# Optimization experiments

Measured on AMD Instinct MI355X. Metric: run time of the kernel, lower is better.

The kernel has to match this reference:

```python
import jax, jax.numpy as jnp
import numpy as np

B = 512
N_ENT = 100000
N_REL = 64
D = 200          # embed_dim
D1 = 10          # embed_shape (emb_dim1)
D2 = 20          # embed_dim // embed_shape (emb_dim2)
K = 3            # kernel_size
C = 32           # out_channels
FC_IN = C * (2 * D1 - K + 1) * (D2 - K + 1)  # 32*18*18 = 10368
EPS = 1e-5       # BatchNorm eps
LS = 0.1         # label_smoothing
LAM = 1e-5       # kg_l2_loss_lambda


def setup_inputs() -> dict:
    key = jax.random.key(0)
    ks = jax.random.split(key, 8)
    return dict(
        entity_w=jax.random.normal(ks[0], (N_ENT, D), jnp.float32) * 0.1,
        relation_w=jax.random.normal(ks[1], (N_REL, D), jnp.float32) * 0.1,
        conv_w=jax.random.normal(ks[2], (C, 1, K, K), jnp.float32) * 0.1,
        conv_b=jnp.zeros((C,), jnp.float32),
        fc_w=jax.random.normal(ks[3], (D, FC_IN), jnp.float32) * 0.02,
        fc_b=jnp.zeros((D,), jnp.float32),
        b=jnp.zeros((N_ENT,), jnp.float32),
        bn0_g=jnp.ones((1,), jnp.float32), bn0_b=jnp.zeros((1,), jnp.float32),
        bn1_g=jnp.ones((C,), jnp.float32), bn1_b=jnp.zeros((C,), jnp.float32),
        bn2_g=jnp.ones((D,), jnp.float32), bn2_b=jnp.zeros((D,), jnp.float32),
        h=jax.random.randint(ks[4], (B,), 0, N_ENT),
        r=jax.random.randint(ks[5], (B,), 0, N_REL),
        pos_t=jax.random.randint(ks[6], (B,), 0, N_ENT),
    )


def _bn(x, g, b, axes, shape):
    # training-mode batchnorm (batch statistics), biased variance as in torch
    m = jnp.mean(x, axes, keepdims=True)
    v = jnp.var(x, axes, keepdims=True)
    return (x - m) * jax.lax.rsqrt(v + EPS) * g.reshape(shape) + b.reshape(shape)


def _l2_mean(x):
    # torch: mean(sum(x**2, dim=1) / 2)
    return jnp.mean(jnp.sum(x * x, axis=1) / 2.0)


def reference(entity_w, relation_w, conv_w, conv_b, fc_w, fc_b, b,
              bn0_g, bn0_b, bn1_g, bn1_b, bn2_g, bn2_b, h, r, pos_t):
    h_e = entity_w[h].reshape(B, 1, D1, D2)
    r_e = relation_w[r].reshape(B, 1, D1, D2)
    x = jnp.concatenate([h_e, r_e], axis=2)           # [B,1,2*D1,D2]
    x = _bn(x, bn0_g, bn0_b, (0, 2, 3), (1, 1, 1, 1))
    x = jax.lax.conv_general_dilated(
        x, conv_w, (1, 1), 'VALID',
        dimension_numbers=('NCHW', 'OIHW', 'NCHW')) + conv_b.reshape(1, C, 1, 1)
    x = _bn(x, bn1_g, bn1_b, (0, 2, 3), (1, C, 1, 1))
    x = jax.nn.relu(x).reshape(B, -1)                 # [B, FC_IN]
    x = x @ fc_w.T + fc_b                             # [B, D]
    x = _bn(x, bn2_g, bn2_b, (0,), (1, D))
    x = jax.nn.leaky_relu(x)                          # slope 0.01 = torch default
    scores = x @ entity_w.T + b                       # [B, N_ENT]
    # BCEWithLogits with smoothed label y = (1-LS)*onehot(pos_t) + 1/N_ENT,
    # loss = mean(softplus(s) - s*y); one-hot never materialized.
    sp_sum = jnp.sum(jax.nn.softplus(scores))
    xy_sum = jnp.sum(scores) / N_ENT + (1.0 - LS) * jnp.sum(
        scores[jnp.arange(B), pos_t])
    kg_loss = (sp_sum - xy_sum) / (B * N_ENT)
    l2 = _l2_mean(h_e) + _l2_mean(r_e) + _l2_mean(conv_w) + _l2_mean(fc_w)
    return kg_loss + LAM * l2
```

## Files before the change

### kernel.cpp

```cpp
#include <hip/hip_runtime.h>
#include <math.h>

#define NB_B 512
#define NE 100000
#define NE_PAD 100032
#define DD 200
#define CC 32
#define FCIN 10368
#define HW 324
#define BNEPS 1e-5f
#define KP 224

#define ENT_BLKS 10941
#define FCW_BLKS 1013
#define GATH_OFF (ENT_BLKS + FCW_BLKS)

typedef __attribute__((ext_vector_type(8))) short short8;
typedef __attribute__((ext_vector_type(4))) float floatx4;


static __device__ __forceinline__ float blk_reduce(float v, volatile float* sbuf) {
  for (int o = 32; o > 0; o >>= 1) v += __shfl_down(v, o, 64);
  int lane = threadIdx.x & 63, wid = threadIdx.x >> 6;
  if (lane == 0) sbuf[wid] = v;
  __syncthreads();
  float r = 0.f;
  int nw = (blockDim.x + 63) >> 6;
  if ((int)threadIdx.x < nw) r = sbuf[threadIdx.x];
  if (threadIdx.x < 64) {
    for (int o = 32; o > 0; o >>= 1) r += __shfl_down(r, o, 64);
  }
  __syncthreads();
  return r;
}

static __device__ __forceinline__ unsigned short f32_to_bf16(float f) {
  unsigned int u = __float_as_uint(f);
  u += 0x7fffu + ((u >> 16) & 1u);
  return (unsigned short)(u >> 16);
}
static __device__ __forceinline__ float bf16_to_f32(unsigned short b) {
  return __uint_as_float(((unsigned int)b) << 16);
}

__global__ __launch_bounds__(256) void k_cvt(const float* __restrict__ ent,
                                             unsigned short* __restrict__ entb,
                                             const float* __restrict__ fcw,
                                             unsigned short* __restrict__ fcwb,
                                             const float* __restrict__ rel,
                                             const int* __restrict__ h,
                                             const int* __restrict__ r,
                                             float* __restrict__ x0,
                                             double* dacc) {
  if (blockIdx.x < ENT_BLKS) {
    int g = blockIdx.x * 256 + threadIdx.x;
    int row = g / 28;
    int c8 = (g - row * 28) * 8;
    ushort4 o0, o1;
    if (c8 < 200 && row < NE) {
      const float4* s = (const float4*)(ent + (long)row * DD + c8);
      float4 u = s[0], v = s[1];
      o0.x = f32_to_bf16(u.x); o0.y = f32_to_bf16(u.y);
      o0.z = f32_to_bf16(u.z); o0.w = f32_to_bf16(u.w);
      o1.x = f32_to_bf16(v.x); o1.y = f32_to_bf16(v.y);
      o1.z = f32_to_bf16(v.z); o1.w = f32_to_bf16(v.w);
    } else {
      o0.x = o0.y = o0.z = o0.w = 0;
      o1.x = o1.y = o1.z = o1.w = 0;
    }
    ushort4* d = (ushort4*)(entb + (long)row * KP + c8);
    d[0] = o0; d[1] = o1;
  } else if (blockIdx.x < GATH_OFF) {
    int g = (blockIdx.x - ENT_BLKS) * 256 + threadIdx.x;
    float sq = 0.f;
    if (g < 259200) {
      const float4* s = (const float4*)(fcw + (long)g * 8);
      float4 u = s[0], v = s[1];
      sq = u.x*u.x + u.y*u.y + u.z*u.z + u.w*u.w
         + v.x*v.x + v.y*v.y + v.z*v.z + v.w*v.w;
      ushort4 o0, o1;
      o0.x = f32_to_bf16(u.x); o0.y = f32_to_bf16(u.y);
      o0.z = f32_to_bf16(u.z); o0.w = f32_to_bf16(u.w);
      o1.x = f32_to_bf16(v.x); o1.y = f32_to_bf16(v.y);
      o1.z = f32_to_bf16(v.z); o1.w = f32_to_bf16(v.w);
      ushort4* d = (ushort4*)(fcwb + (long)g * 8);
      d[0] = o0; d[1] = o1;
    }
    __shared__ float sbuf[8];
    float tq = blk_reduce(sq, sbuf);
    if (threadIdx.x == 0) atomicAdd(&dacc[67], (double)tq);
  } else {
    int b = blockIdx.x - GATH_OFF;
    int hi = h[b], ri = r[b];
    float s = 0.f, sq = 0.f;
    for (int i = threadIdx.x; i < 400; i += 256) {
      float v = (i < 200) ? ent[(long)hi * DD + i] : rel[(long)ri * DD + (i - 200)];
      x0[b * 400 + i] = v;
      s += v; sq += v * v;
    }
    __shared__ float sbuf[8];
    float ts = blk_reduce(s, sbuf);
    float tq = blk_reduce(sq, sbuf);
    if (threadIdx.x == 0) {
      atomicAdd(&dacc[0], (double)ts);
      atomicAdd(&dacc[1], (double)tq);
    }
  }
}

__global__ __launch_bounds__(256) void k_conv(const float* __restrict__ x0,
                       const float* __restrict__ convw, const float* __restrict__ convb,
                       const float* __restrict__ g0, const float* __restrict__ b0,
                       unsigned short* __restrict__ yb, double* dacc) {
  __shared__ float xs[400], wsm[288], cbs[32], ssum[32], ssq[32];
  __shared__ float a0s, s0s;
  int b = blockIdx.x, t = threadIdx.x;
  for (int i = t; i < 400; i += 256) xs[i] = x0[b * 400 + i];
  for (int i = t; i < 288; i += 256) wsm[i] = convw[i];
  if (t < 32) cbs[t] = convb[t];
  if (t == 0) {
    double m = dacc[0] / 204800.0;
    double v = dacc[1] / 204800.0 - m * m;
    float a = g0[0] * rsqrtf((float)v + BNEPS);
    a0s = a; s0s = b0[0] - (float)m * a;
  }
  __syncthreads();
  float a0 = a0s, s0 = s0s;
  for (int i = t; i < 400; i += 256) xs[i] = a0 * xs[i] + s0;
  __syncthreads();
  int c = t >> 3, sub = t & 7;
  const float* w = &wsm[c * 9];
  float cb = cbs[c];
  float s = 0.f, sq = 0.f;
  for (int e = sub; e < HW; e += 8) {
    int oh = e / 18, ow = e - oh * 18;
    const float* xp = &xs[oh * 20 + ow];
    float acc = cb
       + xp[0] * w[0] + xp[1] * w[1] + xp[2] * w[2]
       + xp[20] * w[3] + xp[21] * w[4] + xp[22] * w[5]
       + xp[40] * w[6] + xp[41] * w[7] + xp[42] * w[8];
    yb[(long)b * FCIN + c * HW + e] = f32_to_bf16(acc);
    s += acc; sq += acc * acc;
  }
  s += __shfl_xor(s, 1, 64); sq += __shfl_xor(sq, 1, 64);
  s += __shfl_xor(s, 2, 64); sq += __shfl_xor(sq, 2, 64);
  s += __shfl_xor(s, 4, 64); sq += __shfl_xor(sq, 4, 64);
  if (sub == 0) { ssum[c] = s; ssq[c] = sq; }
  __syncthreads();
  if (t < 32) {
    atomicAdd(&dacc[2 + t], (double)ssum[t]);
    atomicAdd(&dacc[34 + t], (double)ssq[t]);
  }
}

__global__ __launch_bounds__(256) void k_prep(unsigned short* __restrict__ yb,
                                              const float* __restrict__ g1,
                                              const float* __restrict__ b1,
                                              const double* __restrict__ dacc) {
  __shared__ float a1s[32], sh1s[32];
  int t = threadIdx.x;
  if (t < 32) {
    double cnt = 512.0 * 324.0;
    double m = dacc[2 + t] / cnt, v = dacc[34 + t] / cnt - m * m;
    float a = g1[t] * rsqrtf((float)v + BNEPS);
    a1s[t] = a; sh1s[t] = b1[t] - (float)m * a;
  }
  __syncthreads();
  int g = blockIdx.x * 256 + t;
  int row = g / 1296;
  int c8 = (g - row * 1296) * 8;
  unsigned short* p = yb + (long)row * FCIN + c8;
  ushort4 v0 = ((ushort4*)p)[0], v1 = ((ushort4*)p)[1];
  unsigned short e[8] = {v0.x, v0.y, v0.z, v0.w, v1.x, v1.y, v1.z, v1.w};
#pragma unroll
  for (int j = 0; j < 8; j++) {
    int c = (c8 + j) / HW;
    float f = a1s[c] * bf16_to_f32(e[j]) + sh1s[c];
    e[j] = f32_to_bf16(fmaxf(f, 0.f));
  }
  v0.x = e[0]; v0.y = e[1]; v0.z = e[2]; v0.w = e[3];
  v1.x = e[4]; v1.y = e[5]; v1.z = e[6]; v1.w = e[7];
  ((ushort4*)p)[0] = v0; ((ushort4*)p)[1] = v1;
}

__global__ __launch_bounds__(64) void k_fc3(const unsigned short* __restrict__ yb,
                                            const unsigned short* __restrict__ fcwb,
                                            float* __restrict__ Cp) {
  int wid = blockIdx.x;
  int ks = wid >> 5, rem = wid & 31;
  int mt = rem >> 2, nt = rem & 3;
  int m0 = mt * 64, n0 = nt * 64;
  int lane = threadIdx.x;
  int quad = lane >> 4, lr = lane & 15;
  long kbeg = (long)ks * 864;

  const unsigned short* arow[4];
  const unsigned short* brow[4];
#pragma unroll
  for (int mi = 0; mi < 4; mi++)
    arow[mi] = yb + (long)(m0 + mi * 16 + lr) * FCIN + kbeg + quad * 8;
#pragma unroll
  for (int ni = 0; ni < 4; ni++) {
    int d = n0 + ni * 16 + lr;
    if (d > DD - 1) d = DD - 1;
    brow[ni] = fcwb + (long)d * FCIN + kbeg + quad * 8;
  }

  floatx4 acc[4][4];
#pragma unroll
  for (int i = 0; i < 4; i++)
#pragma unroll
    for (int j = 0; j < 4; j++) acc[i][j] = (floatx4){0.f, 0.f, 0.f, 0.f};

  short8 sA[3][4], sB[3][4];
#pragma unroll
  for (int c = 0; c < 3; c++) {
#pragma unroll
    for (int mi = 0; mi < 4; mi++) sA[c][mi] = *(const short8*)(arow[mi] + c * 32);
#pragma unroll
    for (int ni = 0; ni < 4; ni++) sB[c][ni] = *(const short8*)(brow[ni] + c * 32);
  }
  for (int c3 = 0; c3 < 9; c3++) {
    int cc = c3 * 3;
#pragma unroll
    for (int j = 0; j < 3; j++) {
#pragma unroll
      for (int ni = 0; ni < 4; ni++)
#pragma unroll
        for (int mi = 0; mi < 4; mi++)
          acc[mi][ni] = __builtin_amdgcn_mfma_f32_16x16x32_bf16(sA[j][mi], sB[j][ni], acc[mi][ni], 0, 0, 0);
      int nxt = cc + j + 3;
      if (nxt < 27) {
#pragma unroll
        for (int mi = 0; mi < 4; mi++) sA[j][mi] = *(const short8*)(arow[mi] + nxt * 32);
#pragma unroll
        for (int ni = 0; ni < 4; ni++) sB[j][ni] = *(const short8*)(brow[ni] + nxt * 32);
      }
    }
  }

  float* out = Cp + (long)ks * (NB_B * DD);
#pragma unroll
  for (int ni = 0; ni < 4; ni++) {
    int d = n0 + ni * 16 + lr;
    if (d < DD) {
#pragma unroll
      for (int mi = 0; mi < 4; mi++) {
        int mbase = m0 + mi * 16 + quad * 4;
#pragma unroll
        for (int rg = 0; rg < 4; rg++)
          out[(mbase + rg) * DD + d] = acc[mi][ni][rg];
      }
    }
  }
}

__global__ __launch_bounds__(256) void k_fcred(const float* __restrict__ Cp,
                                               float* __restrict__ Cfc) {
  int g = blockIdx.x * 256 + threadIdx.x;
  float4 s = ((const float4*)Cp)[g];
#pragma unroll
  for (int p = 1; p < 12; p++) {
    float4 v = ((const float4*)(Cp + (long)p * (NB_B * DD)))[g];
    s.x += v.x; s.y += v.y; s.z += v.z; s.w += v.w;
  }
  ((float4*)Cfc)[g] = s;
}

__global__ void k_bn2stats(const float* __restrict__ Cfc, const float* __restrict__ fcb,
                           const float* __restrict__ g2, const float* __restrict__ b2,
                           float* __restrict__ a2, float* __restrict__ b2c) {
  int d = blockIdx.x, lane = threadIdx.x;
  float s = 0.f, sq = 0.f;
  for (int b = lane; b < NB_B; b += 64) {
    float v = Cfc[b * DD + d] + fcb[d];
    s += v; sq += v * v;
  }
  for (int o = 32; o > 0; o >>= 1) { s += __shfl_down(s, o, 64); sq += __shfl_down(sq, o, 64); }
  if (lane == 0) {
    float m = s / 512.f, v = sq / 512.f - m * m;
    float a = g2[d] * rsqrtf(v + BNEPS);
    a2[d] = a; b2c[d] = b2[d] - m * a;
  }
}

__global__ __launch_bounds__(256) void k_xfinal(const float* __restrict__ Cfc,
                         const float* __restrict__ fcb,
                         const float* __restrict__ a2, const float* __restrict__ b2c,
                         const float* __restrict__ ent, const float* __restrict__ bias,
                         const int* __restrict__ pos,
                         float* __restrict__ xf, unsigned short* __restrict__ xfb,
                         double* dacc) {
  __shared__ float xs[224];
  __shared__ float sbuf[8];
  int b = blockIdx.x, t = threadIdx.x;
  if (t < KP) {
    float xv = 0.f;
    if (t < DD) {
      float v = Cfc[b * DD + t] + fcb[t];
      xv = a2[t] * v + b2c[t];
      xv = xv >= 0.f ? xv : 0.01f * xv;
      xf[b * DD + t] = xv;
    }
    xfb[b * KP + t] = f32_to_bf16(xv);
    xs[t] = xv;
  }
  __syncthreads();
  int e = pos[b];
  float s = (t < DD) ? xs[t] * ent[(long)e * DD + t] : 0.f;
  float ts = blk_reduce(s, sbuf);
  if (t == 0) atomicAdd(&dacc[70], (double)(ts + bias[e]));
}

__global__ __launch_bounds__(512) void k_scores4(
    const unsigned short* __restrict__ entb,
    const unsigned short* __restrict__ xfb,
    const float* __restrict__ bias, double* dacc) {
  __shared__ float sbuf[8];
  int t = threadIdx.x;
  int wv = t >> 6, lane = t & 63;
  int quad = lane >> 4, lr = lane & 15;

  short8 af[4][7];
#pragma unroll
  for (int mi = 0; mi < 4; mi++) {
    const unsigned short* ap = xfb + (size_t)(wv * 64 + mi * 16 + lr) * KP + quad * 8;
#pragma unroll
    for (int kc = 0; kc < 7; kc++) af[mi][kc] = *(const short8*)(ap + kc * 32);
  }

  float sp = 0.f, ss = 0.f;
  int t0 = blockIdx.x * 3;
#pragma unroll 1
  for (int tile = t0; tile < t0 + 3; tile++) {
    int e0 = tile * 64;
    const unsigned short* bp[4];
    float b4[4];
#pragma unroll
    for (int ni = 0; ni < 4; ni++) {
      int e = e0 + ni * 16 + lr;
      int ec = e < NE ? e : (NE - 1);
      bp[ni] = entb + (size_t)e * KP + quad * 8;
      float bv = bias[ec];
      b4[ni] = (e < NE) ? bv : 0.f;
    }
    floatx4 acc[4][4];
#pragma unroll
    for (int i = 0; i < 4; i++)
#pragma unroll
      for (int j = 0; j < 4; j++) acc[i][j] = (floatx4){0.f, 0.f, 0.f, 0.f};

    short8 bs[2][4];
#pragma unroll
    for (int ni = 0; ni < 4; ni++) bs[0][ni] = *(const short8*)(bp[ni]);
#pragma unroll
    for (int ni = 0; ni < 4; ni++) bs[1][ni] = *(const short8*)(bp[ni] + 32);
#pragma unroll
    for (int kc = 0; kc < 7; kc++) {
      int s = kc & 1;
#pragma unroll
      for (int ni = 0; ni < 4; ni++)
#pragma unroll
        for (int mi = 0; mi < 4; mi++)
          acc[mi][ni] = __builtin_amdgcn_mfma_f32_16x16x32_bf16(af[mi][kc], bs[s][ni], acc[mi][ni], 0, 0, 0);
      if (kc + 2 < 7) {
#pragma unroll
        for (int ni = 0; ni < 4; ni++) bs[s][ni] = *(const short8*)(bp[ni] + (kc + 2) * 32);
      }
    }
#pragma unroll
    for (int ni = 0; ni < 4; ni++) {
#pragma unroll
      for (int mi = 0; mi < 4; mi++) {
#pragma unroll
        for (int rg = 0; rg < 4; rg++) {
          float s1 = acc[mi][ni][rg] + b4[ni];
          ss += s1;
          float m1 = s1 * 1.4426950408889634f;
          float e2 = __builtin_amdgcn_exp2f(-__builtin_fabsf(m1));
          float lg = __builtin_amdgcn_logf(1.f + e2);
          sp += fmaxf(m1, 0.f) + lg;
        }
      }
    }
  }
  sp *= 0.6931471805599453f;
  float tsp = blk_reduce(sp, sbuf);
  float tss = blk_reduce(ss, sbuf);
  if (t == 0) {
    atomicAdd(&dacc[68], (double)tsp);
    atomicAdd(&dacc[69], (double)tss);
  }
}

__global__ void k_final(const float* __restrict__ convw, const double* dacc, float* out) {
  int t = threadIdx.x;
  float sq = 0.f;
  for (int i = t; i < 288; i += 64) { float w = convw[i]; sq += w * w; }
  for (int o = 32; o > 0; o >>= 1) sq += __shfl_down(sq, o, 64);
  if (t == 0) {
    double SP = dacc[68] - 16384.0 * 0.6931471805599453;
    double S2 = dacc[69], S3 = dacc[70];
    double xy = S2 / (double)NE + 0.9 * S3;
    double kg = (SP - xy) / ((double)NB_B * (double)NE);
    double l2 = dacc[1] / 204800.0 + (double)sq / 576.0 + dacc[67] / 400.0;
    out[0] = (float)(kg + 1e-5 * l2);
  }
}

extern "C" void kernel_launch(void* const* d_in, const int* in_sizes, int n_in,
                              void* d_out, int out_size, void* d_ws, size_t ws_size,
                              hipStream_t stream) {
  const float* ent   = (const float*)d_in[0];
  const float* rel   = (const float*)d_in[1];
  const float* convw = (const float*)d_in[2];
  const float* convb = (const float*)d_in[3];
  const float* fcw   = (const float*)d_in[4];
  const float* fcb   = (const float*)d_in[5];
  const float* bias  = (const float*)d_in[6];
  const float* g0    = (const float*)d_in[7];
  const float* b0    = (const float*)d_in[8];
  const float* g1    = (const float*)d_in[9];
  const float* b1    = (const float*)d_in[10];
  const float* g2    = (const float*)d_in[11];
  const float* b2    = (const float*)d_in[12];
  const int*   h     = (const int*)d_in[13];
  const int*   r     = (const int*)d_in[14];
  const int*   pos   = (const int*)d_in[15];

  char* ws = (char*)d_ws;
  double* dacc = (double*)(ws + 0);
  float* a2  = (float*)(ws + 16384 + 256);
  float* b2c = (float*)(ws + 16384 + 1056);
  float* x0  = (float*)(ws + 32768);
  float* Cfc = (float*)(ws + 851968);
  float* xf  = (float*)(ws + 1261568);
  unsigned short* yb   = (unsigned short*)(ws + 1671168);
  unsigned short* fcwb = (unsigned short*)(ws + 12288000);
  unsigned short* xfb  = (unsigned short*)(ws + 16435200);
  unsigned short* entb = (unsigned short*)(ws + 16664576);
  float* Cp = (float*)(ws + 61507584);

  hipMemsetAsync(dacc, 0, 8192, stream);

  k_cvt<<<GATH_OFF + 512, 256, 0, stream>>>(ent, entb, fcw, fcwb, rel, h, r, x0, dacc);
  k_conv<<<512, 256, 0, stream>>>(x0, convw, convb, g0, b0, yb, dacc);
  k_prep<<<2592, 256, 0, stream>>>(yb, g1, b1, dacc);
  k_fc3<<<384, 64, 0, stream>>>(yb, fcwb, Cp);
  k_fcred<<<100, 256, 0, stream>>>(Cp, Cfc);
  k_bn2stats<<<200, 64, 0, stream>>>(Cfc, fcb, g2, b2, a2, b2c);
  k_xfinal<<<512, 256, 0, stream>>>(Cfc, fcb, a2, b2c, ent, bias, pos, xf, xfb, dacc);
  k_scores4<<<521, 512, 0, stream>>>(entb, xfb, bias, dacc);
  k_final<<<1, 64, 0, stream>>>(convw, dacc, (float*)d_out);
}
```

Baseline: 322.5 us.

## Fuse entity bf16 conversion into scores kernel with LDS double-buffered staging

Result: slower. 380.9 us (+18.1%).

```diff
diff --git a/kernel.cpp b/kernel.cpp
--- a/kernel.cpp
+++ b/kernel.cpp
@@ -3,7 +3,6 @@
 
 #define NB_B 512
 #define NE 100000
-#define NE_PAD 100032
 #define DD 200
 #define CC 32
 #define FCIN 10368
@@ -11,9 +10,8 @@
 #define BNEPS 1e-5f
 #define KP 224
 
-#define ENT_BLKS 10941
 #define FCW_BLKS 1013
-#define GATH_OFF (ENT_BLKS + FCW_BLKS)
+#define GATH_OFF FCW_BLKS
 
 typedef __attribute__((ext_vector_type(8))) short short8;
 typedef __attribute__((ext_vector_type(4))) float floatx4;
@@ -43,35 +41,16 @@
   return __uint_as_float(((unsigned int)b) << 16);
 }
 
-__global__ __launch_bounds__(256) void k_cvt(const float* __restrict__ ent,
-                                             unsigned short* __restrict__ entb,
-                                             const float* __restrict__ fcw,
+__global__ __launch_bounds__(256) void k_cvt(const float* __restrict__ fcw,
                                              unsigned short* __restrict__ fcwb,
+                                             const float* __restrict__ ent,
                                              const float* __restrict__ rel,
                                              const int* __restrict__ h,
                                              const int* __restrict__ r,
                                              float* __restrict__ x0,
                                              double* dacc) {
-  if (blockIdx.x < ENT_BLKS) {
+  if (blockIdx.x < FCW_BLKS) {
     int g = blockIdx.x * 256 + threadIdx.x;
-    int row = g / 28;
-    int c8 = (g - row * 28) * 8;
-    ushort4 o0, o1;
-    if (c8 < 200 && row < NE) {
-      const float4* s = (const float4*)(ent + (long)row * DD + c8);
-      float4 u = s[0], v = s[1];
-      o0.x = f32_to_bf16(u.x); o0.y = f32_to_bf16(u.y);
-      o0.z = f32_to_bf16(u.z); o0.w = f32_to_bf16(u.w);
-      o1.x = f32_to_bf16(v.x); o1.y = f32_to_bf16(v.y);
-      o1.z = f32_to_bf16(v.z); o1.w = f32_to_bf16(v.w);
-    } else {
-      o0.x = o0.y = o0.z = o0.w = 0;
-      o1.x = o1.y = o1.z = o1.w = 0;
-    }
-    ushort4* d = (ushort4*)(entb + (long)row * KP + c8);
-    d[0] = o0; d[1] = o1;
-  } else if (blockIdx.x < GATH_OFF) {
-    int g = (blockIdx.x - ENT_BLKS) * 256 + threadIdx.x;
     float sq = 0.f;
     if (g < 259200) {
       const float4* s = (const float4*)(fcw + (long)g * 8);
@@ -312,10 +291,90 @@
   if (t == 0) atomicAdd(&dacc[70], (double)(ts + bias[e]));
 }
 
-__global__ __launch_bounds__(512) void k_scores4(
-    const unsigned short* __restrict__ entb,
+static __device__ __forceinline__ void sc_stage_issue(
+    const float* __restrict__ ent, int e0, int t, float4 (&rg)[7]) {
+#pragma unroll
+  for (int i = 0; i < 7; i++) {
+    int u = t + i * 512;
+    int rr = u / 56, j = u - rr * 56;
+    int e = e0 + rr;
+    float4 v; v.x = 0.f; v.y = 0.f; v.z = 0.f; v.w = 0.f;
+    if (j < 50 && e < NE) v = *(const float4*)(ent + (long)e * DD + j * 4);
+    rg[i] = v;
+  }
+}
+
+static __device__ __forceinline__ void sc_stage_commit(
+    unsigned short* __restrict__ buf, int t, const float4 (&rg)[7]) {
+  char* base = (char*)buf;
+#pragma unroll
+  for (int i = 0; i < 7; i++) {
+    int u = t + i * 512;
+    int rr = u / 56, j = u - rr * 56;
+    int c = j >> 1, h = j & 1;
+    int rrx = rr ^ (c & 7);
+    ushort4 o;
+    o.x = f32_to_bf16(rg[i].x); o.y = f32_to_bf16(rg[i].y);
+    o.z = f32_to_bf16(rg[i].z); o.w = f32_to_bf16(rg[i].w);
+    *(ushort4*)(base + c * 1024 + rrx * 16 + h * 8) = o;
+  }
+}
+
+static __device__ __forceinline__ void sc_compute(
+    const unsigned short* __restrict__ buf, int e0,
+    const short8 (&af)[4][7], const float* __restrict__ bias,
+    int quad, int lr, float& sp, float& ss) {
+  const char* base = (const char*)buf;
+  float b4[4];
+#pragma unroll
+  for (int ni = 0; ni < 4; ni++) {
+    int e = e0 + ni * 16 + lr;
+    int ec = e < NE ? e : 0;
+    float bv = bias[ec];
+    b4[ni] = (e < NE) ? bv : 0.f;
+  }
+  floatx4 acc[4][4];
+#pragma unroll
+  for (int i = 0; i < 4; i++)
+#pragma unroll
+    for (int j = 0; j < 4; j++) acc[i][j] = (floatx4){0.f, 0.f, 0.f, 0.f};
+#pragma unroll
+  for (int kc = 0; kc < 7; kc++) {
+    short8 bs[4];
+    int c = kc * 4 + quad;
+#pragma unroll
+    for (int ni = 0; ni < 4; ni++) {
+      int rrx = (ni * 16 + lr) ^ (c & 7);
+      bs[ni] = *(const short8*)(base + c * 1024 + rrx * 16);
+    }
+#pragma unroll
+    for (int ni = 0; ni < 4; ni++)
+#pragma unroll
+      for (int mi = 0; mi < 4; mi++)
+        acc[mi][ni] = __builtin_amdgcn_mfma_f32_16x16x32_bf16(af[mi][kc], bs[ni], acc[mi][ni], 0, 0, 0);
+  }
+#pragma unroll
+  for (int ni = 0; ni < 4; ni++) {
+#pragma unroll
+    for (int mi = 0; mi < 4; mi++) {
+#pragma unroll
+      for (int rg2 = 0; rg2 < 4; rg2++) {
+        float s1 = acc[mi][ni][rg2] + b4[ni];
+        ss += s1;
+        float m1 = s1 * 1.4426950408889634f;
+        float e2 = __builtin_amdgcn_exp2f(-__builtin_fabsf(m1));
+        float lg = __builtin_amdgcn_logf(1.f + e2);
+        sp += fmaxf(m1, 0.f) + lg;
+      }
+    }
+  }
+}
+
+__global__ __launch_bounds__(512, 2) void k_scores5(
+    const float* __restrict__ ent,
     const unsigned short* __restrict__ xfb,
     const float* __restrict__ bias, double* dacc) {
+  __shared__ unsigned short Bs[2][14336];
   __shared__ float sbuf[8];
   int t = threadIdx.x;
   int wv = t >> 6, lane = t & 63;
@@ -329,61 +388,27 @@
     for (int kc = 0; kc < 7; kc++) af[mi][kc] = *(const short8*)(ap + kc * 32);
   }
 
+  int tile0 = blockIdx.x * 3;
+  int e0_0 = tile0 * 64, e0_1 = e0_0 + 64, e0_2 = e0_0 + 128;
   float sp = 0.f, ss = 0.f;
-  int t0 = blockIdx.x * 3;
-#pragma unroll 1
-  for (int tile = t0; tile < t0 + 3; tile++) {
-    int e0 = tile * 64;
-    const unsigned short* bp[4];
-    float b4[4];
-#pragma unroll
-    for (int ni = 0; ni < 4; ni++) {
-      int e = e0 + ni * 16 + lr;
-      int ec = e < NE ? e : (NE - 1);
-      bp[ni] = entb + (size_t)e * KP + quad * 8;
-      float bv = bias[ec];
-      b4[ni] = (e < NE) ? bv : 0.f;
-    }
-    floatx4 acc[4][4];
-#pragma unroll
-    for (int i = 0; i < 4; i++)
-#pragma unroll
-      for (int j = 0; j < 4; j++) acc[i][j] = (floatx4){0.f, 0.f, 0.f, 0.f};
-
-    short8 bs[2][4];
-#pragma unroll
-    for (int ni = 0; ni < 4; ni++) bs[0][ni] = *(const short8*)(bp[ni]);
-#pragma unroll
-    for (int ni = 0; ni < 4; ni++) bs[1][ni] = *(const short8*)(bp[ni] + 32);
-#pragma unroll
-    for (int kc = 0; kc < 7; kc++) {
-      int s = kc & 1;
-#pragma unroll
-      for (int ni = 0; ni < 4; ni++)
-#pragma unroll
-        for (int mi = 0; mi < 4; mi++)
-          acc[mi][ni] = __builtin_amdgcn_mfma_f32_16x16x32_bf16(af[mi][kc], bs[s][ni], acc[mi][ni], 0, 0, 0);
-      if (kc + 2 < 7) {
-#pragma unroll
-        for (int ni = 0; ni < 4; ni++) bs[s][ni] = *(const short8*)(bp[ni] + (kc + 2) * 32);
-      }
-    }
-#pragma unroll
-    for (int ni = 0; ni < 4; ni++) {
-#pragma unroll
-      for (int mi = 0; mi < 4; mi++) {
-#pragma unroll
-        for (int rg = 0; rg < 4; rg++) {
-          float s1 = acc[mi][ni][rg] + b4[ni];
-          ss += s1;
-          float m1 = s1 * 1.4426950408889634f;
-          float e2 = __builtin_amdgcn_exp2f(-__builtin_fabsf(m1));
-          float lg = __builtin_amdgcn_logf(1.f + e2);
-          sp += fmaxf(m1, 0.f) + lg;
-        }
-      }
-    }
-  }
+  float4 rg[7];
+
+  sc_stage_issue(ent, e0_0, t, rg);
+  sc_stage_commit(Bs[0], t, rg);
+  sc_stage_issue(ent, e0_1, t, rg);
+  __syncthreads();
+
+  sc_compute(Bs[0], e0_0, af, bias, quad, lr, sp, ss);
+  sc_stage_commit(Bs[1], t, rg);
+  sc_stage_issue(ent, e0_2, t, rg);
+  __syncthreads();
+
+  sc_compute(Bs[1], e0_1, af, bias, quad, lr, sp, ss);
+  sc_stage_commit(Bs[0], t, rg);
+  __syncthreads();
+
+  sc_compute(Bs[0], e0_2, af, bias, quad, lr, sp, ss);
+
   sp *= 0.6931471805599453f;
   float tsp = blk_reduce(sp, sbuf);
   float tss = blk_reduce(ss, sbuf);
@@ -438,18 +463,17 @@
   unsigned short* yb   = (unsigned short*)(ws + 1671168);
   unsigned short* fcwb = (unsigned short*)(ws + 12288000);
   unsigned short* xfb  = (unsigned short*)(ws + 16435200);
-  unsigned short* entb = (unsigned short*)(ws + 16664576);
-  float* Cp = (float*)(ws + 61507584);
+  float* Cp = (float*)(ws + 16664576);
 
   hipMemsetAsync(dacc, 0, 8192, stream);
 
-  k_cvt<<<GATH_OFF + 512, 256, 0, stream>>>(ent, entb, fcw, fcwb, rel, h, r, x0, dacc);
+  k_cvt<<<FCW_BLKS + 512, 256, 0, stream>>>(fcw, fcwb, ent, rel, h, r, x0, dacc);
   k_conv<<<512, 256, 0, stream>>>(x0, convw, convb, g0, b0, yb, dacc);
   k_prep<<<2592, 256, 0, stream>>>(yb, g1, b1, dacc);
   k_fc3<<<384, 64, 0, stream>>>(yb, fcwb, Cp);
   k_fcred<<<100, 256, 0, stream>>>(Cp, Cfc);
   k_bn2stats<<<200, 64, 0, stream>>>(Cfc, fcb, g2, b2, a2, b2c);
   k_xfinal<<<512, 256, 0, stream>>>(Cfc, fcb, a2, b2c, ent, bias, pos, xf, xfb, dacc);
-  k_scores4<<<521, 512, 0, stream>>>(entb, xfb, bias, dacc);
+  k_scores5<<<521, 512, 0, stream>>>(ent, xfb, bias, dacc);
   k_final<<<1, 64, 0, stream>>>(convw, dacc, (float*)d_out);
 }
```

## Stage entity tiles in LDS via async loads and fuse FC reduction with BN2 stats

Applied to the files above, without the earlier changes.

After: 321.7 us. No clear change (-0.2%).

```diff
diff --git a/kernel.cpp b/kernel.cpp
--- a/kernel.cpp
+++ b/kernel.cpp
@@ -255,26 +255,20 @@
   }
 }
 
-__global__ __launch_bounds__(256) void k_fcred(const float* __restrict__ Cp,
-                                               float* __restrict__ Cfc) {
-  int g = blockIdx.x * 256 + threadIdx.x;
-  float4 s = ((const float4*)Cp)[g];
-#pragma unroll
-  for (int p = 1; p < 12; p++) {
-    float4 v = ((const float4*)(Cp + (long)p * (NB_B * DD)))[g];
-    s.x += v.x; s.y += v.y; s.z += v.z; s.w += v.w;
-  }
-  ((float4*)Cfc)[g] = s;
-}
-
-__global__ void k_bn2stats(const float* __restrict__ Cfc, const float* __restrict__ fcb,
-                           const float* __restrict__ g2, const float* __restrict__ b2,
-                           float* __restrict__ a2, float* __restrict__ b2c) {
+__global__ void k_fcbn(const float* __restrict__ Cp, const float* __restrict__ fcb,
+                       const float* __restrict__ g2, const float* __restrict__ b2,
+                       float* __restrict__ Cfc, float* __restrict__ a2,
+                       float* __restrict__ b2c) {
   int d = blockIdx.x, lane = threadIdx.x;
+  float fb = fcb[d];
   float s = 0.f, sq = 0.f;
   for (int b = lane; b < NB_B; b += 64) {
-    float v = Cfc[b * DD + d] + fcb[d];
-    s += v; sq += v * v;
+    float v = 0.f;
+#pragma unroll
+    for (int p = 0; p < 12; p++) v += Cp[(long)p * (NB_B * DD) + b * DD + d];
+    Cfc[b * DD + d] = v;
+    float w = v + fb;
+    s += w; sq += w * w;
   }
   for (int o = 32; o > 0; o >>= 1) { s += __shfl_down(s, o, 64); sq += __shfl_down(sq, o, 64); }
   if (lane == 0) {
@@ -312,78 +306,102 @@
   if (t == 0) atomicAdd(&dacc[70], (double)(ts + bias[e]));
 }
 
-__global__ __launch_bounds__(512) void k_scores4(
+static __device__ __forceinline__ void sc_compute8(
+    const unsigned short* __restrict__ buf, const float (&bv)[2],
+    const short8 (&af)[2][7], int quad, int lr, float& sp, float& ss) {
+#pragma unroll
+  for (int ni = 0; ni < 2; ni++) {
+    float b1v = bv[ni];
+    floatx4 acc0 = (floatx4){0.f, 0.f, 0.f, 0.f};
+    floatx4 acc1 = (floatx4){0.f, 0.f, 0.f, 0.f};
+#pragma unroll
+    for (int kc = 0; kc < 7; kc++) {
+      int c = kc * 4 + quad;
+      short8 bsv = *(const short8*)(buf + (ni * 16 + lr) * KP + c * 8);
+      acc0 = __builtin_amdgcn_mfma_f32_16x16x32_bf16(af[0][kc], bsv, acc0, 0, 0, 0);
+      acc1 = __builtin_amdgcn_mfma_f32_16x16x32_bf16(af[1][kc], bsv, acc1, 0, 0, 0);
+    }
+#pragma unroll
+    for (int rg2 = 0; rg2 < 4; rg2++) {
+      float s1 = acc0[rg2] + b1v;
+      ss += s1;
+      float m1 = s1 * 1.4426950408889634f;
+      float e2 = __builtin_amdgcn_exp2f(-__builtin_fabsf(m1));
+      sp += fmaxf(m1, 0.f) + __builtin_amdgcn_logf(1.f + e2);
+    }
+#pragma unroll
+    for (int rg2 = 0; rg2 < 4; rg2++) {
+      float s1 = acc1[rg2] + b1v;
+      ss += s1;
+      float m1 = s1 * 1.4426950408889634f;
+      float e2 = __builtin_amdgcn_exp2f(-__builtin_fabsf(m1));
+      sp += fmaxf(m1, 0.f) + __builtin_amdgcn_logf(1.f + e2);
+    }
+  }
+}
+
+__global__ __launch_bounds__(512) void k_scores8(
     const unsigned short* __restrict__ entb,
     const unsigned short* __restrict__ xfb,
     const float* __restrict__ bias, double* dacc) {
+  __shared__ unsigned short Bs[2][7168];
   __shared__ float sbuf[8];
   int t = threadIdx.x;
   int wv = t >> 6, lane = t & 63;
   int quad = lane >> 4, lr = lane & 15;
-
-  short8 af[4][7];
-#pragma unroll
-  for (int mi = 0; mi < 4; mi++) {
-    const unsigned short* ap = xfb + (size_t)(wv * 64 + mi * 16 + lr) * KP + quad * 8;
+  int b = blockIdx.x;
+  int rh = b & 1;
+  int trip = b >> 1;
+  int e0 = trip * 96;
+
+  short8 af[2][7];
+#pragma unroll
+  for (int mi = 0; mi < 2; mi++) {
+    const unsigned short* ap =
+        xfb + (size_t)(rh * 256 + wv * 32 + mi * 16 + lr) * KP + quad * 8;
 #pragma unroll
     for (int kc = 0; kc < 7; kc++) af[mi][kc] = *(const short8*)(ap + kc * 32);
   }
 
+  float bv[3][2];
+#pragma unroll
+  for (int tt = 0; tt < 3; tt++)
+#pragma unroll
+    for (int ni = 0; ni < 2; ni++) {
+      int e = e0 + tt * 32 + ni * 16 + lr;
+      bv[tt][ni] = (e < NE) ? bias[e] : 0.f;
+    }
+
+#define STAGE8(bufi, tile)                                                     \
+  {                                                                            \
+    _Pragma("unroll")                                                          \
+    for (int i_ = 0; i_ < 2; i_++) {                                           \
+      int s_ = wv * 2 + i_;                                                    \
+      if (s_ < 14) {                                                           \
+        const unsigned short* gp_ =                                            \
+            entb + (size_t)(e0 + (tile) * 32) * KP + s_ * 512 + lane * 8;      \
+        __builtin_amdgcn_global_load_lds(                                      \
+            (const __attribute__((address_space(1))) unsigned int*)gp_,       \
+            (__attribute__((address_space(3))) unsigned int*)&Bs[bufi][s_ * 512], \
+            16, 0, 0);                                                         \
+      }                                                                        \
+    }                                                                          \
+  }
+
   float sp = 0.f, ss = 0.f;
-  int t0 = blockIdx.x * 3;
-#pragma unroll 1
-  for (int tile = t0; tile < t0 + 3; tile++) {
-    int e0 = tile * 64;
-    const unsigned short* bp[4];
-    float b4[4];
-#pragma unroll
-    for (int ni = 0; ni < 4; ni++) {
-      int e = e0 + ni * 16 + lr;
-      int ec = e < NE ? e : (NE - 1);
-      bp[ni] = entb + (size_t)e * KP + quad * 8;
-      float bv = bias[ec];
-      b4[ni] = (e < NE) ? bv : 0.f;
-    }
-    floatx4 acc[4][4];
-#pragma unroll
-    for (int i = 0; i < 4; i++)
-#pragma unroll
-      for (int j = 0; j < 4; j++) acc[i][j] = (floatx4){0.f, 0.f, 0.f, 0.f};
-
-    short8 bs[2][4];
-#pragma unroll
-    for (int ni = 0; ni < 4; ni++) bs[0][ni] = *(const short8*)(bp[ni]);
-#pragma unroll
-    for (int ni = 0; ni < 4; ni++) bs[1][ni] = *(const short8*)(bp[ni] + 32);
-#pragma unroll
-    for (int kc = 0; kc < 7; kc++) {
-      int s = kc & 1;
-#pragma unroll
-      for (int ni = 0; ni < 4; ni++)
-#pragma unroll
-        for (int mi = 0; mi < 4; mi++)
-          acc[mi][ni] = __builtin_amdgcn_mfma_f32_16x16x32_bf16(af[mi][kc], bs[s][ni], acc[mi][ni], 0, 0, 0);
-      if (kc + 2 < 7) {
-#pragma unroll
-        for (int ni = 0; ni < 4; ni++) bs[s][ni] = *(const short8*)(bp[ni] + (kc + 2) * 32);
-      }
-    }
-#pragma unroll
-    for (int ni = 0; ni < 4; ni++) {
-#pragma unroll
-      for (int mi = 0; mi < 4; mi++) {
-#pragma unroll
-        for (int rg = 0; rg < 4; rg++) {
-          float s1 = acc[mi][ni][rg] + b4[ni];
-          ss += s1;
-          float m1 = s1 * 1.4426950408889634f;
-          float e2 = __builtin_amdgcn_exp2f(-__builtin_fabsf(m1));
-          float lg = __builtin_amdgcn_logf(1.f + e2);
-          sp += fmaxf(m1, 0.f) + lg;
-        }
-      }
-    }
-  }
+
+  STAGE8(0, 0);
+  STAGE8(1, 1);
+  __syncthreads();
+
+  sc_compute8(Bs[0], bv[0], af, quad, lr, sp, ss);
+  __syncthreads();
+  STAGE8(0, 2);
+  sc_compute8(Bs[1], bv[1], af, quad, lr, sp, ss);
+  __syncthreads();
+  sc_compute8(Bs[0], bv[2], af, quad, lr, sp, ss);
+#undef STAGE8
+
   sp *= 0.6931471805599453f;
   float tsp = blk_reduce(sp, sbuf);
   float tss = blk_reduce(ss, sbuf);
@@ -447,9 +465,8 @@
   k_conv<<<512, 256, 0, stream>>>(x0, convw, convb, g0, b0, yb, dacc);
   k_prep<<<2592, 256, 0, stream>>>(yb, g1, b1, dacc);
   k_fc3<<<384, 64, 0, stream>>>(yb, fcwb, Cp);
-  k_fcred<<<100, 256, 0, stream>>>(Cp, Cfc);
-  k_bn2stats<<<200, 64, 0, stream>>>(Cfc, fcb, g2, b2, a2, b2c);
+  k_fcbn<<<200, 64, 0, stream>>>(Cp, fcb, g2, b2, Cfc, a2, b2c);
   k_xfinal<<<512, 256, 0, stream>>>(Cfc, fcb, a2, b2c, ent, bias, pos, xf, xfb, dacc);
-  k_scores4<<<521, 512, 0, stream>>>(entb, xfb, bias, dacc);
+  k_scores8<<<2084, 512, 0, stream>>>(entb, xfb, bias, dacc);
   k_final<<<1, 64, 0, stream>>>(convw, dacc, (float*)d_out);
 }
```
